# Optimization experiments

Hardware: AMD Instinct MI355X
Metric: run time of the kernel (lower is better)

The kernel has to match this reference:

```python
import jax, jax.numpy as jnp
import numpy as np

EPS = 1e-5


def gated_graph_conv(x, edge_index, W, w_ih, w_hh, b_ih, b_hh):
    # W: [num_layers, C, C]; PyG pads input features up to out_channels C.
    N = x.shape[0]
    C = W.shape[1]
    if x.shape[1] < C:
        x = jnp.pad(x, ((0, 0), (0, C - x.shape[1])))
    src, dst = edge_index[0], edge_index[1]
    for i in range(W.shape[0]):
        m = x @ W[i]                                   # [N, C]
        agg = jax.ops.segment_sum(m[src], dst, num_segments=N)  # scatter-add aggr
        # GRUCell(agg, x)
        gi = agg @ w_ih.T + b_ih                       # [N, 3C]
        gh = x @ w_hh.T + b_hh
        ir, iz, in_ = jnp.split(gi, 3, axis=-1)
        hr, hz, hn = jnp.split(gh, 3, axis=-1)
        r = jax.nn.sigmoid(ir + hr)
        z = jax.nn.sigmoid(iz + hz)
        n = jnp.tanh(in_ + r * hn)
        x = (1.0 - z) * n + z * x
    return x


def batch_norm_eval(x, gamma, beta, mean, var):
    return (x - mean) * jax.lax.rsqrt(var + EPS) * gamma + beta


def _ggc_params(key, C):
    ks = jax.random.split(key, 5)
    s = 1.0 / np.sqrt(C)
    return (jax.random.uniform(ks[0], (4, C, C), minval=-s, maxval=s),
            jax.random.uniform(ks[1], (3 * C, C), minval=-s, maxval=s),
            jax.random.uniform(ks[2], (3 * C, C), minval=-s, maxval=s),
            jax.random.uniform(ks[3], (3 * C,), minval=-s, maxval=s),
            jax.random.uniform(ks[4], (3 * C,), minval=-s, maxval=s))


def _bn_params(key, C):
    ks = jax.random.split(key, 4)
    return (jax.random.normal(ks[0], (C,)) * 0.1 + 1.0,
            jax.random.normal(ks[1], (C,)) * 0.1,
            jax.random.normal(ks[2], (C,)) * 0.1,
            jax.random.uniform(ks[3], (C,), minval=0.5, maxval=1.5))


def setup_inputs() -> dict:
    key = jax.random.key(0)
    N, E, NF, NG, NA = 50000, 800000, 32, 256, 10
    ks = jax.random.split(key, 12)
    x = jax.random.normal(ks[0], (N, NF), dtype=jnp.float32)
    edge_index = jax.random.randint(ks[1], (2, E), 0, N, dtype=jnp.int64)
    batch = jnp.sort(jax.random.randint(ks[2], (N,), 0, NG, dtype=jnp.int64))
    c1 = _ggc_params(ks[3], NF)
    c2 = _ggc_params(ks[4], 64)
    c3 = _ggc_params(ks[5], 128)
    bn1 = _bn_params(ks[6], NF)
    bn2 = _bn_params(ks[7], 64)
    s1 = 1.0 / np.sqrt(128)
    fc1_W = jax.random.uniform(ks[8], (256, 128), minval=-s1, maxval=s1)
    fc1_b = jax.random.uniform(ks[9], (256,), minval=-s1, maxval=s1)
    s2 = 1.0 / np.sqrt(256)
    fc2_W = jax.random.uniform(ks[10], (NA, 256), minval=-s2, maxval=s2)
    fc2_b = jax.random.uniform(ks[11], (NA,), minval=-s2, maxval=s2)
    d = {"x": x, "edge_index": edge_index, "batch": batch,
         "fc1_W": fc1_W, "fc1_b": fc1_b, "fc2_W": fc2_W, "fc2_b": fc2_b}
    for name, p in (("conv1", c1), ("conv2", c2), ("conv3", c3)):
        d[name + "_W"], d[name + "_wih"], d[name + "_whh"], d[name + "_bih"], d[name + "_bhh"] = p
    for name, p in (("bn1", bn1), ("bn2", bn2)):
        d[name + "_gamma"], d[name + "_beta"], d[name + "_mean"], d[name + "_var"] = p
    return d


def reference(x, edge_index, batch,
              conv1_W, conv1_wih, conv1_whh, conv1_bih, conv1_bhh,
              conv2_W, conv2_wih, conv2_whh, conv2_bih, conv2_bhh,
              conv3_W, conv3_wih, conv3_whh, conv3_bih, conv3_bhh,
              bn1_gamma, bn1_beta, bn1_mean, bn1_var,
              bn2_gamma, bn2_beta, bn2_mean, bn2_var,
              fc1_W, fc1_b, fc2_W, fc2_b):
    NUM_GRAPHS = 256
    h = jax.nn.elu(gated_graph_conv(x, edge_index, conv1_W, conv1_wih, conv1_whh, conv1_bih, conv1_bhh))
    h = batch_norm_eval(h, bn1_gamma, bn1_beta, bn1_mean, bn1_var)
    h = jax.nn.elu(gated_graph_conv(h, edge_index, conv2_W, conv2_wih, conv2_whh, conv2_bih, conv2_bhh))
    h = batch_norm_eval(h, bn2_gamma, bn2_beta, bn2_mean, bn2_var)
    h = jax.nn.elu(gated_graph_conv(h, edge_index, conv3_W, conv3_wih, conv3_whh, conv3_bih, conv3_bhh))
    g = jax.ops.segment_sum(h, batch, num_segments=NUM_GRAPHS)  # global_add_pool
    g = jax.nn.elu(g @ fc1_W.T + fc1_b)
    # dropout is identity in eval mode
    return jax.nn.log_softmax(g @ fc2_W.T + fc2_b, axis=-1)
```

## Files before the change

### kernel.cpp

```cpp
#include <hip/hip_runtime.h>
#include <math.h>


#define EPS_BN 1e-5f

typedef short short8 __attribute__((ext_vector_type(8)));
typedef unsigned short u16x8 __attribute__((ext_vector_type(8)));
typedef float f32x4 __attribute__((ext_vector_type(4)));

__device__ __forceinline__ float elu_f(float v) {
    return v > 0.f ? v : expm1f(v);
}
__device__ __forceinline__ float sigmoid_f(float v) {
    return 1.f / (1.f + __expf(-v));
}
__device__ __forceinline__ float tanh_f(float v) {
    float e = __expf(2.f * v);
    return 1.f - 2.f / (e + 1.f);
}
__device__ __forceinline__ unsigned short f2bf(float f) {
    unsigned u = __float_as_uint(f);
    unsigned r = (u + 0x7FFF + ((u >> 16) & 1)) >> 16;
    return (unsigned short)r;
}
__device__ __forceinline__ float bf2f(unsigned short b) {
    return __uint_as_float(((unsigned)b) << 16);
}
__device__ __forceinline__ void put_hl(unsigned short* __restrict__ hi,
                                       unsigned short* __restrict__ lo,
                                       size_t idx, float v) {
    unsigned short h = f2bf(v);
    hi[idx] = h;
    lo[idx] = f2bf(v - bf2f(h));
}


__global__ __launch_bounds__(256) void hist_kernel(
    const int* __restrict__ ei, int* __restrict__ deg, int E) {
    int e = blockIdx.x * 256 + threadIdx.x;
    if (e < E) atomicAdd(&deg[ei[E + e]], 1);
}

__global__ __launch_bounds__(256) void scan1_kernel(
    const int* __restrict__ deg, int* __restrict__ out,
    int* __restrict__ blockSums, int N) {
    __shared__ int sdata[256];
    int b = blockIdx.x, t = threadIdx.x;
    int base = b * 1024 + t * 4;
    int v[4], s = 0;
#pragma unroll
    for (int i = 0; i < 4; ++i) {
        v[i] = (base + i < N) ? deg[base + i] : 0;
        s += v[i];
    }
    sdata[t] = s;
    __syncthreads();
    for (int off = 1; off < 256; off <<= 1) {
        int x = (t >= off) ? sdata[t - off] : 0;
        __syncthreads();
        sdata[t] += x;
        __syncthreads();
    }
    int run = sdata[t] - s;
#pragma unroll
    for (int i = 0; i < 4; ++i) {
        if (base + i < N) out[base + i] = run;
        run += v[i];
    }
    if (t == 255) blockSums[b] = sdata[255];
}

__global__ void scan2_kernel(int* blockSums, int nb) {
    if (threadIdx.x == 0 && blockIdx.x == 0) {
        int run = 0;
        for (int i = 0; i < nb; ++i) {
            int v = blockSums[i];
            blockSums[i] = run;
            run += v;
        }
    }
}

__global__ __launch_bounds__(256) void scan3_kernel(
    const int* __restrict__ out, const int* __restrict__ blockSums,
    int* __restrict__ rowstart, int* __restrict__ writeptr, int N, int E) {
    int i = blockIdx.x * 256 + threadIdx.x;
    if (i < N) {
        int v = out[i] + blockSums[i >> 10];
        rowstart[i] = v;
        writeptr[i] = v;
    }
    if (i == 0) rowstart[N] = E;
}

__global__ __launch_bounds__(256) void fill_kernel(
    const int* __restrict__ ei, int* __restrict__ writeptr,
    int* __restrict__ csr_src, int E) {
    int e = blockIdx.x * 256 + threadIdx.x;
    if (e < E) {
        int d = ei[E + e];
        int p = atomicAdd(&writeptr[d], 1);
        csr_src[p] = ei[e];
    }
}


template <int C>
__global__ __launch_bounds__(256) void wc_kernel(
    const float* __restrict__ W, const float* __restrict__ wih,
    float* __restrict__ Wc) {
    int idx = blockIdx.x * 256 + threadIdx.x;
    if (idx >= 4 * C * 3 * C) return;
    int l = idx / (C * 3 * C);
    int r = idx % (C * 3 * C);
    int k = r / (3 * C);
    int row = r % (3 * C);
    const float* wrow = W + ((size_t)l * C + k) * C;
    const float* irow = wih + (size_t)row * C;
    float acc = 0.f;
#pragma unroll 4
    for (int t = 0; t < C; ++t) acc += wrow[t] * irow[t];
    Wc[idx] = acc;
}


template <int C>
__global__ __launch_bounds__(256) void swizzle_b2_kernel(
    const float* __restrict__ Wc, const float* __restrict__ whh,
    unsigned short* __restrict__ BsHi, unsigned short* __restrict__ BsLo) {
    constexpr int CT = C / 16;
    int idx = blockIdx.x * 256 + threadIdx.x;
    if (idx >= 4 * 6 * C * C) return;
    int l = idx / (6 * C * C);
    int r0 = idx % (6 * C * C);
    int j = r0 & 7;
    int lane = (r0 >> 3) & 63;
    int rest = r0 >> 9;
    int tslot = rest % (3 * CT);
    int ks = rest / (3 * CT);
    int k = ks * 32 + (lane >> 4) * 8 + j;
    int g = tslot / CT;
    int lt = tslot % CT;
    int c = lt * 16 + (lane & 15);
    int row = g * C + c;
    float v = (k < C) ? Wc[((size_t)l * C + k) * 3 * C + row]
                      : whh[(size_t)row * C + (k - C)];
    unsigned short h = f2bf(v);
    BsHi[idx] = h;
    BsLo[idx] = f2bf(v - bf2f(h));
}


template <int C>
__global__ __launch_bounds__(256) void gather_kernel(
    const unsigned short* __restrict__ Xhi,
    const int* __restrict__ rowstart, const int* __restrict__ csr_src,
    unsigned short* __restrict__ Shi, int N) {
    constexpr int LPG = C / 8;
    constexpr int GPB = 256 / LPG;
    int lane = threadIdx.x % LPG;
    int grp = threadIdx.x / LPG;
    int d = blockIdx.x * GPB + grp;
    if (d >= N) return;
    int p = rowstart[d];
    int p1 = rowstart[d + 1];
    float a[8];
#pragma unroll
    for (int j = 0; j < 8; ++j) a[j] = 0.f;
    int off = lane * 8;
    for (; p + 3 < p1; p += 4) {
        int s0 = csr_src[p];
        int s1 = csr_src[p + 1];
        int s2 = csr_src[p + 2];
        int s3 = csr_src[p + 3];
        u16x8 h0 = *(const u16x8*)(Xhi + (size_t)s0 * C + off);
        u16x8 h1 = *(const u16x8*)(Xhi + (size_t)s1 * C + off);
        u16x8 h2 = *(const u16x8*)(Xhi + (size_t)s2 * C + off);
        u16x8 h3 = *(const u16x8*)(Xhi + (size_t)s3 * C + off);
#pragma unroll
        for (int j = 0; j < 8; ++j) {
            a[j] += (bf2f(h0[j]) + bf2f(h1[j])) + (bf2f(h2[j]) + bf2f(h3[j]));
        }
    }
    for (; p < p1; ++p) {
        int s0 = csr_src[p];
        u16x8 h0 = *(const u16x8*)(Xhi + (size_t)s0 * C + off);
#pragma unroll
        for (int j = 0; j < 8; ++j) a[j] += bf2f(h0[j]);
    }
    size_t base = (size_t)d * C + off;
#pragma unroll
    for (int j = 0; j < 8; ++j) Shi[base + j] = f2bf(a[j]);
}


template <int C, int NT, int MINW>
__global__ __launch_bounds__(256, MINW) void gru_mfma_kernel(
    const unsigned short* __restrict__ HinHi, const unsigned short* __restrict__ HinLo,
    unsigned short* __restrict__ HoutHi, unsigned short* __restrict__ HoutLo,
    const unsigned short* __restrict__ Shi,
    const unsigned short* __restrict__ BsHi, const unsigned short* __restrict__ BsLo,
    const float* __restrict__ biasI, const float* __restrict__ biasH, int N) {
    constexpr int CT = C / 16;
    constexpr int KS = C / 16;
    constexpr int CTW = CT / 4;
    constexpr int TPW = NT / 16;
    int wave = threadIdx.x >> 6;
    int lane = threadIdx.x & 63;
    int quad = lane >> 4;
    int l16 = lane & 15;
    int node0 = blockIdx.x * NT;
    int arow[TPW];
#pragma unroll
    for (int t = 0; t < TPW; ++t) {
        int r = node0 + t * 16 + l16;
        arow[t] = r < N ? r : N - 1;
    }
    f32x4 accR[CTW][TPW], accZ[CTW][TPW], accN[CTW][TPW], accH[CTW][TPW];
#pragma unroll
    for (int ct = 0; ct < CTW; ++ct)
#pragma unroll
        for (int t = 0; t < TPW; ++t) {
            accR[ct][t] = (f32x4){0.f, 0.f, 0.f, 0.f};
            accZ[ct][t] = (f32x4){0.f, 0.f, 0.f, 0.f};
            accN[ct][t] = (f32x4){0.f, 0.f, 0.f, 0.f};
            accH[ct][t] = (f32x4){0.f, 0.f, 0.f, 0.f};
        }
    const short8* bhi = (const short8*)BsHi;
    const short8* blo = (const short8*)BsLo;

    for (int ks = 0; ks < KS / 2; ++ks) {
        int k0 = ks * 32 + quad * 8;
        short8 ahi[TPW];
#pragma unroll
        for (int t = 0; t < TPW; ++t)
            ahi[t] = *(const short8*)(Shi + (size_t)arow[t] * C + k0);
#pragma unroll
        for (int ct = 0; ct < CTW; ++ct) {
            int ts = ks * 3 * CT + wave * CTW + ct;
            short8 bhf = bhi[(size_t)ts * 64 + lane];
            short8 blf = blo[(size_t)ts * 64 + lane];
#pragma unroll
            for (int t = 0; t < TPW; ++t) {
                accR[ct][t] = __builtin_amdgcn_mfma_f32_16x16x32_bf16(ahi[t], bhf, accR[ct][t], 0, 0, 0);
                accR[ct][t] = __builtin_amdgcn_mfma_f32_16x16x32_bf16(ahi[t], blf, accR[ct][t], 0, 0, 0);
            }
            bhf = bhi[(size_t)(ts + CT) * 64 + lane];
            blf = blo[(size_t)(ts + CT) * 64 + lane];
#pragma unroll
            for (int t = 0; t < TPW; ++t) {
                accZ[ct][t] = __builtin_amdgcn_mfma_f32_16x16x32_bf16(ahi[t], bhf, accZ[ct][t], 0, 0, 0);
                accZ[ct][t] = __builtin_amdgcn_mfma_f32_16x16x32_bf16(ahi[t], blf, accZ[ct][t], 0, 0, 0);
            }
            bhf = bhi[(size_t)(ts + 2 * CT) * 64 + lane];
            blf = blo[(size_t)(ts + 2 * CT) * 64 + lane];
#pragma unroll
            for (int t = 0; t < TPW; ++t) {
                accN[ct][t] = __builtin_amdgcn_mfma_f32_16x16x32_bf16(ahi[t], bhf, accN[ct][t], 0, 0, 0);
                accN[ct][t] = __builtin_amdgcn_mfma_f32_16x16x32_bf16(ahi[t], blf, accN[ct][t], 0, 0, 0);
            }
        }
    }
    for (int ks = KS / 2; ks < KS; ++ks) {
        int k0 = ks * 32 + quad * 8 - C;
        short8 ahi[TPW], alo[TPW];
#pragma unroll
        for (int t = 0; t < TPW; ++t) {
            ahi[t] = *(const short8*)(HinHi + (size_t)arow[t] * C + k0);
            alo[t] = *(const short8*)(HinLo + (size_t)arow[t] * C + k0);
        }
#pragma unroll
        for (int ct = 0; ct < CTW; ++ct) {
            int ts = ks * 3 * CT + wave * CTW + ct;
            short8 bhf = bhi[(size_t)ts * 64 + lane];
            short8 blf = blo[(size_t)ts * 64 + lane];
#pragma unroll
            for (int t = 0; t < TPW; ++t) {
                accR[ct][t] = __builtin_amdgcn_mfma_f32_16x16x32_bf16(ahi[t], bhf, accR[ct][t], 0, 0, 0);
                accR[ct][t] = __builtin_amdgcn_mfma_f32_16x16x32_bf16(alo[t], bhf, accR[ct][t], 0, 0, 0);
                accR[ct][t] = __builtin_amdgcn_mfma_f32_16x16x32_bf16(ahi[t], blf, accR[ct][t], 0, 0, 0);
            }
            bhf = bhi[(size_t)(ts + CT) * 64 + lane];
            blf = blo[(size_t)(ts + CT) * 64 + lane];
#pragma unroll
            for (int t = 0; t < TPW; ++t) {
                accZ[ct][t] = __builtin_amdgcn_mfma_f32_16x16x32_bf16(ahi[t], bhf, accZ[ct][t], 0, 0, 0);
                accZ[ct][t] = __builtin_amdgcn_mfma_f32_16x16x32_bf16(alo[t], bhf, accZ[ct][t], 0, 0, 0);
                accZ[ct][t] = __builtin_amdgcn_mfma_f32_16x16x32_bf16(ahi[t], blf, accZ[ct][t], 0, 0, 0);
            }
            bhf = bhi[(size_t)(ts + 2 * CT) * 64 + lane];
            blf = blo[(size_t)(ts + 2 * CT) * 64 + lane];
#pragma unroll
            for (int t = 0; t < TPW; ++t) {
                accH[ct][t] = __builtin_amdgcn_mfma_f32_16x16x32_bf16(ahi[t], bhf, accH[ct][t], 0, 0, 0);
                accH[ct][t] = __builtin_amdgcn_mfma_f32_16x16x32_bf16(alo[t], bhf, accH[ct][t], 0, 0, 0);
                accH[ct][t] = __builtin_amdgcn_mfma_f32_16x16x32_bf16(ahi[t], blf, accH[ct][t], 0, 0, 0);
            }
        }
    }

#pragma unroll
    for (int ct = 0; ct < CTW; ++ct) {
        int c = (wave * CTW + ct) * 16 + l16;
        float bir = biasI[c], biz = biasI[C + c], bin = biasI[2 * C + c];
        float bhr = biasH[c], bhz = biasH[C + c], bhn = biasH[2 * C + c];
#pragma unroll
        for (int t = 0; t < TPW; ++t) {
#pragma unroll
            for (int r = 0; r < 4; ++r) {
                int node = node0 + t * 16 + quad * 4 + r;
                if (node < N) {
                    size_t gi = (size_t)node * C + c;
                    float xo = bf2f(HinHi[gi]) + bf2f(HinLo[gi]);
                    float rv = sigmoid_f(accR[ct][t][r] + bir + bhr);
                    float zv = sigmoid_f(accZ[ct][t][r] + biz + bhz);
                    float nv = tanh_f(accN[ct][t][r] + bin + rv * (accH[ct][t][r] + bhn));
                    put_hl(HoutHi, HoutLo, gi, (1.f - zv) * nv + zv * xo);
                }
            }
        }
    }
}

__global__ __launch_bounds__(256, 4) void gru32_kernel(
    const unsigned short* __restrict__ HinHi, const unsigned short* __restrict__ HinLo,
    unsigned short* __restrict__ HoutHi, unsigned short* __restrict__ HoutLo,
    const unsigned short* __restrict__ Shi,
    const unsigned short* __restrict__ BsHi, const unsigned short* __restrict__ BsLo,
    const float* __restrict__ biasI, const float* __restrict__ biasH, int N) {
    constexpr int C = 32;
    constexpr int CT = 2;
    int wave = threadIdx.x >> 6;
    int lane = threadIdx.x & 63;
    int quad = lane >> 4;
    int l16 = lane & 15;
    int node0 = blockIdx.x * 64 + wave * 16;
    int ar = node0 + l16;
    if (ar >= N) ar = N - 1;
    f32x4 accR[CT], accZ[CT], accN[CT], accH[CT];
#pragma unroll
    for (int t = 0; t < CT; ++t) {
        accR[t] = (f32x4){0.f, 0.f, 0.f, 0.f};
        accZ[t] = (f32x4){0.f, 0.f, 0.f, 0.f};
        accN[t] = (f32x4){0.f, 0.f, 0.f, 0.f};
        accH[t] = (f32x4){0.f, 0.f, 0.f, 0.f};
    }
    const short8* bhi = (const short8*)BsHi;
    const short8* blo = (const short8*)BsLo;
    int k0 = quad * 8;
    {
        short8 ahi = *(const short8*)(Shi + (size_t)ar * C + k0);
#pragma unroll
        for (int g = 0; g < 3; ++g) {
            f32x4* acc = g == 0 ? accR : (g == 1 ? accZ : accN);
#pragma unroll
            for (int t = 0; t < CT; ++t) {
                int ts = g * CT + t;
                short8 bhf = bhi[(size_t)ts * 64 + lane];
                short8 blf = blo[(size_t)ts * 64 + lane];
                acc[t] = __builtin_amdgcn_mfma_f32_16x16x32_bf16(ahi, bhf, acc[t], 0, 0, 0);
                acc[t] = __builtin_amdgcn_mfma_f32_16x16x32_bf16(ahi, blf, acc[t], 0, 0, 0);
            }
        }
    }
    {
        short8 ahi = *(const short8*)(HinHi + (size_t)ar * C + k0);
        short8 alo = *(const short8*)(HinLo + (size_t)ar * C + k0);
#pragma unroll
        for (int g = 0; g < 3; ++g) {
            f32x4* acc = g == 0 ? accR : (g == 1 ? accZ : accH);
#pragma unroll
            for (int t = 0; t < CT; ++t) {
                int ts = 3 * CT + g * CT + t;
                short8 bhf = bhi[(size_t)ts * 64 + lane];
                short8 blf = blo[(size_t)ts * 64 + lane];
                acc[t] = __builtin_amdgcn_mfma_f32_16x16x32_bf16(ahi, bhf, acc[t], 0, 0, 0);
                acc[t] = __builtin_amdgcn_mfma_f32_16x16x32_bf16(alo, bhf, acc[t], 0, 0, 0);
                acc[t] = __builtin_amdgcn_mfma_f32_16x16x32_bf16(ahi, blf, acc[t], 0, 0, 0);
            }
        }
    }
#pragma unroll
    for (int t = 0; t < CT; ++t) {
        int c = t * 16 + l16;
        float bir = biasI[c], biz = biasI[C + c], bin = biasI[2 * C + c];
        float bhr = biasH[c], bhz = biasH[C + c], bhn = biasH[2 * C + c];
#pragma unroll
        for (int r = 0; r < 4; ++r) {
            int node = node0 + quad * 4 + r;
            if (node < N) {
                size_t gi = (size_t)node * C + c;
                float xo = bf2f(HinHi[gi]) + bf2f(HinLo[gi]);
                float rv = sigmoid_f(accR[t][r] + bir + bhr);
                float zv = sigmoid_f(accZ[t][r] + biz + bhz);
                float nv = tanh_f(accN[t][r] + bin + rv * (accH[t][r] + bhn));
                put_hl(HoutHi, HoutLo, gi, (1.f - zv) * nv + zv * xo);
            }
        }
    }
}


__global__ __launch_bounds__(256) void init_x_kernel(
    const float* __restrict__ x, unsigned short* __restrict__ Hhi,
    unsigned short* __restrict__ Hlo, int total) {
    int t = blockIdx.x * 256 + threadIdx.x;
    if (t < total) put_hl(Hhi, Hlo, t, x[t]);
}

template <int Cin, int Cout>
__global__ __launch_bounds__(256) void elu_bn_pad_kernel(
    const unsigned short* __restrict__ Shi, const unsigned short* __restrict__ Slo,
    unsigned short* __restrict__ Dhi, unsigned short* __restrict__ Dlo,
    const float* __restrict__ gamma, const float* __restrict__ beta,
    const float* __restrict__ mean, const float* __restrict__ var, int N) {
    long t = (long)blockIdx.x * 256 + threadIdx.x;
    long total = (long)N * Cout;
    if (t >= total) return;
    int n = (int)(t / Cout);
    int c = (int)(t & (Cout - 1));
    float v = 0.f;
    if (c < Cin) {
        size_t si = (size_t)n * Cin + c;
        float x = bf2f(Shi[si]) + bf2f(Slo[si]);
        x = elu_f(x);
        v = (x - mean[c]) * rsqrtf(var[c] + EPS_BN) * gamma[c] + beta[c];
    }
    put_hl(Dhi, Dlo, t, v);
}

__global__ __launch_bounds__(256) void pool_elu_kernel(
    const unsigned short* __restrict__ Hhi, const unsigned short* __restrict__ Hlo,
    const int* __restrict__ batch, float* __restrict__ G, int N) {
    long t = (long)blockIdx.x * 256 + threadIdx.x;
    if (t >= (long)N * 128) return;
    int n = (int)(t >> 7);
    int c = (int)(t & 127);
    float v = elu_f(bf2f(Hhi[t]) + bf2f(Hlo[t]));
    atomicAdd(&G[batch[n] * 128 + c], v);
}

__global__ __launch_bounds__(256) void fc1_kernel(
    const float* __restrict__ G, const float* __restrict__ W,
    const float* __restrict__ b, float* __restrict__ G2) {
    __shared__ float row[128];
    int g = blockIdx.x;
    int j = threadIdx.x;
    if (j < 128) row[j] = G[g * 128 + j];
    __syncthreads();
    float acc = b[j];
    for (int k = 0; k < 128; ++k) acc += row[k] * W[j * 128 + k];
    G2[g * 256 + j] = elu_f(acc);
}

__global__ __launch_bounds__(64) void fc2_logsoftmax_kernel(
    const float* __restrict__ G2, const float* __restrict__ W,
    const float* __restrict__ b, float* __restrict__ out) {
    __shared__ float row[256];
    __shared__ float logits[10];
    __shared__ float red[2];
    int g = blockIdx.x;
    int tid = threadIdx.x;
    for (int i = tid; i < 256; i += 64) row[i] = G2[g * 256 + i];
    __syncthreads();
    if (tid < 10) {
        float acc = b[tid];
        for (int k = 0; k < 256; ++k) acc += row[k] * W[tid * 256 + k];
        logits[tid] = acc;
    }
    __syncthreads();
    if (tid == 0) {
        float m = -1e30f;
        for (int a = 0; a < 10; ++a) m = fmaxf(m, logits[a]);
        float s = 0.f;
        for (int a = 0; a < 10; ++a) s += expf(logits[a] - m);
        red[0] = m;
        red[1] = logf(s);
    }
    __syncthreads();
    if (tid < 10) out[g * 10 + tid] = logits[tid] - red[0] - red[1];
}


template <int C>
static void run_conv(unsigned short* Ahi, unsigned short* Alo,
                     unsigned short* Bhi, unsigned short* Blo,
                     unsigned short* Shi,
                     float* Wc, unsigned short* BsHi, unsigned short* BsLo,
                     const float* W, const float* wih, const float* whh,
                     const float* bih, const float* bhh,
                     const int* rowstart, const int* csr_src,
                     int N, int E, hipStream_t stream) {
    wc_kernel<C><<<(4 * C * 3 * C + 255) / 256, 256, 0, stream>>>(W, wih, Wc);
    swizzle_b2_kernel<C><<<(4 * 6 * C * C + 255) / 256, 256, 0, stream>>>(Wc, whh, BsHi, BsLo);
    constexpr int NT = (C == 128) ? 32 : 64;
    int nb = (N + NT - 1) / NT;
    constexpr int GPB = 2048 / C;
    int gblocks = (N + GPB - 1) / GPB;
    unsigned short *inHi = Ahi, *inLo = Alo, *outHi = Bhi, *outLo = Blo;
    for (int it = 0; it < 4; ++it) {
        gather_kernel<C><<<gblocks, 256, 0, stream>>>(
            inHi, rowstart, csr_src, Shi, N);
        const unsigned short* bs_h = BsHi + (size_t)it * 6 * C * C;
        const unsigned short* bs_l = BsLo + (size_t)it * 6 * C * C;
        if constexpr (C == 32)
            gru32_kernel<<<nb, 256, 0, stream>>>(
                inHi, inLo, outHi, outLo, Shi, bs_h, bs_l, bih, bhh, N);
        else
            gru_mfma_kernel<C, NT, 3><<<nb, 256, 0, stream>>>(
                inHi, inLo, outHi, outLo, Shi, bs_h, bs_l, bih, bhh, N);
        unsigned short* tp;
        tp = inHi; inHi = outHi; outHi = tp;
        tp = inLo; inLo = outLo; outLo = tp;
    }
}

extern "C" void kernel_launch(void* const* d_in, const int* in_sizes, int n_in,
                              void* d_out, int out_size, void* d_ws, size_t ws_size,
                              hipStream_t stream) {
    const float* x = (const float*)d_in[0];
    const int* ei = (const int*)d_in[1];
    const int* batch = (const int*)d_in[2];
    const float* fc1W = (const float*)d_in[3];
    const float* fc1b = (const float*)d_in[4];
    const float* fc2W = (const float*)d_in[5];
    const float* fc2b = (const float*)d_in[6];
    const float* c1W = (const float*)d_in[7];
    const float* c1wih = (const float*)d_in[8];
    const float* c1whh = (const float*)d_in[9];
    const float* c1bih = (const float*)d_in[10];
    const float* c1bhh = (const float*)d_in[11];
    const float* c2W = (const float*)d_in[12];
    const float* c2wih = (const float*)d_in[13];
    const float* c2whh = (const float*)d_in[14];
    const float* c2bih = (const float*)d_in[15];
    const float* c2bhh = (const float*)d_in[16];
    const float* c3W = (const float*)d_in[17];
    const float* c3wih = (const float*)d_in[18];
    const float* c3whh = (const float*)d_in[19];
    const float* c3bih = (const float*)d_in[20];
    const float* c3bhh = (const float*)d_in[21];
    const float* bn1g = (const float*)d_in[22];
    const float* bn1b = (const float*)d_in[23];
    const float* bn1m = (const float*)d_in[24];
    const float* bn1v = (const float*)d_in[25];
    const float* bn2g = (const float*)d_in[26];
    const float* bn2b = (const float*)d_in[27];
    const float* bn2m = (const float*)d_in[28];
    const float* bn2v = (const float*)d_in[29];

    int N = in_sizes[0] / 32;
    int E = in_sizes[1] / 2;

    const size_t NB = (size_t)N * 128;
    unsigned short* PAhi = (unsigned short*)d_ws;
    unsigned short* PAlo = PAhi + NB;
    unsigned short* PBhi = PAlo + NB;
    unsigned short* PBlo = PBhi + NB;
    unsigned short* Shi = PBlo + NB;
    unsigned short* Slo = Shi + NB;
    unsigned short* BsHi = Slo + NB;
    unsigned short* BsLo = BsHi + 393216;
    float* Wc = (float*)(BsLo + 393216);
    float* G = Wc + 196608;
    float* G2 = G + 32768;
    int* deg = (int*)(G2 + 65536);
    int* scanout = deg + N;
    int* rowstart = scanout + N;
    int* writeptr = rowstart + N + 1;
    int* blockSums = writeptr + N;
    int* csr_src = blockSums + 64;

    hipMemsetAsync(deg, 0, (size_t)N * sizeof(int), stream);
    int eblocks = (E + 255) / 256;
    hist_kernel<<<eblocks, 256, 0, stream>>>(ei, deg, E);
    int nscan = (N + 1023) / 1024;
    scan1_kernel<<<nscan, 256, 0, stream>>>(deg, scanout, blockSums, N);
    scan2_kernel<<<1, 64, 0, stream>>>(blockSums, nscan);
    scan3_kernel<<<(N + 255) / 256, 256, 0, stream>>>(scanout, blockSums, rowstart, writeptr, N, E);
    fill_kernel<<<eblocks, 256, 0, stream>>>(ei, writeptr, csr_src, E);

    init_x_kernel<<<(N * 32 + 255) / 256, 256, 0, stream>>>(x, PAhi, PAlo, N * 32);

    run_conv<32>(PAhi, PAlo, PBhi, PBlo, Shi, Wc, BsHi, BsLo,
                 c1W, c1wih, c1whh, c1bih, c1bhh, rowstart, csr_src, N, E, stream);
    elu_bn_pad_kernel<32, 64><<<(int)(((long)N * 64 + 255) / 256), 256, 0, stream>>>(
        PAhi, PAlo, PBhi, PBlo, bn1g, bn1b, bn1m, bn1v, N);

    run_conv<64>(PBhi, PBlo, PAhi, PAlo, Shi, Wc, BsHi, BsLo,
                 c2W, c2wih, c2whh, c2bih, c2bhh, rowstart, csr_src, N, E, stream);
    elu_bn_pad_kernel<64, 128><<<(int)(((long)N * 128 + 255) / 256), 256, 0, stream>>>(
        PBhi, PBlo, PAhi, PAlo, bn2g, bn2b, bn2m, bn2v, N);

    run_conv<128>(PAhi, PAlo, PBhi, PBlo, Shi, Wc, BsHi, BsLo,
                  c3W, c3wih, c3whh, c3bih, c3bhh, rowstart, csr_src, N, E, stream);

    hipMemsetAsync(G, 0, 256 * 128 * sizeof(float), stream);
    pool_elu_kernel<<<(int)(((long)N * 128 + 255) / 256), 256, 0, stream>>>(
        PAhi, PAlo, batch, G, N);

    fc1_kernel<<<256, 256, 0, stream>>>(G, fc1W, fc1b, G2);
    fc2_logsoftmax_kernel<<<256, 64, 0, stream>>>(G2, fc2W, fc2b, (float*)d_out);
}
```

Baseline: 931.0 us.

## Software-pipeline B and A fragment loads in GRU MFMA kernel, retune tiles

Flattens the two k-loops of the GRU MFMA kernel into one fully unrolled loop. B fragments are prefetched three steps ahead through a four-slot register ring, and the A rows for the next k-step are double-buffered, so global load latency overlaps with MFMA work. It also fixes the node tile at 32 for C=64, which was 64 before, and raises min waves per EU to 4 for C=64. The gru32 launch grid is kept unchanged. The cost is higher register pressure and more blocks, with a risk of spills or lower occupancy.

After: 935.1 us. No clear change (+0.4%).

```diff
diff --git a/kernel.cpp b/kernel.cpp
--- a/kernel.cpp
+++ b/kernel.cpp
@@ -194,17 +194,20 @@
 }
 
 
-template <int C, int NT, int MINW>
+template <int C, int MINW>
 __global__ __launch_bounds__(256, MINW) void gru_mfma_kernel(
     const unsigned short* __restrict__ HinHi, const unsigned short* __restrict__ HinLo,
     unsigned short* __restrict__ HoutHi, unsigned short* __restrict__ HoutLo,
     const unsigned short* __restrict__ Shi,
     const unsigned short* __restrict__ BsHi, const unsigned short* __restrict__ BsLo,
     const float* __restrict__ biasI, const float* __restrict__ biasH, int N) {
+    constexpr int NT = 32;
     constexpr int CT = C / 16;
     constexpr int KS = C / 16;
     constexpr int CTW = CT / 4;
     constexpr int TPW = NT / 16;
+    constexpr int JPK = CTW * 3;
+    constexpr int JT = KS * JPK;
     int wave = threadIdx.x >> 6;
     int lane = threadIdx.x & 63;
     int quad = lane >> 4;
@@ -229,72 +232,65 @@
     const short8* bhi = (const short8*)BsHi;
     const short8* blo = (const short8*)BsLo;
 
-    for (int ks = 0; ks < KS / 2; ++ks) {
-        int k0 = ks * 32 + quad * 8;
-        short8 ahi[TPW];
-#pragma unroll
-        for (int t = 0; t < TPW; ++t)
-            ahi[t] = *(const short8*)(Shi + (size_t)arow[t] * C + k0);
-#pragma unroll
-        for (int ct = 0; ct < CTW; ++ct) {
-            int ts = ks * 3 * CT + wave * CTW + ct;
-            short8 bhf = bhi[(size_t)ts * 64 + lane];
-            short8 blf = blo[(size_t)ts * 64 + lane];
+    short8 bufh[4], bufl[4];
+    short8 ahiP[2][TPW], aloP[2][TPW];
+
+    auto loadB = [&](int j) {
+        int ks = j / JPK;
+        int rr = j % JPK;
+        int ct = rr / 3;
+        int g = rr % 3;
+        size_t ts = (size_t)(ks * 3 * CT + wave * CTW + ct + g * CT);
+        bufh[j & 3] = bhi[ts * 64 + lane];
+        bufl[j & 3] = blo[ts * 64 + lane];
+    };
+    auto loadA = [&](int ks) {
+        int slot = ks & 1;
+        if (ks < KS / 2) {
+            int k0 = ks * 32 + quad * 8;
+#pragma unroll
+            for (int t = 0; t < TPW; ++t)
+                ahiP[slot][t] = *(const short8*)(Shi + (size_t)arow[t] * C + k0);
+        } else {
+            int k0 = ks * 32 + quad * 8 - C;
 #pragma unroll
             for (int t = 0; t < TPW; ++t) {
-                accR[ct][t] = __builtin_amdgcn_mfma_f32_16x16x32_bf16(ahi[t], bhf, accR[ct][t], 0, 0, 0);
-                accR[ct][t] = __builtin_amdgcn_mfma_f32_16x16x32_bf16(ahi[t], blf, accR[ct][t], 0, 0, 0);
+                ahiP[slot][t] = *(const short8*)(HinHi + (size_t)arow[t] * C + k0);
+                aloP[slot][t] = *(const short8*)(HinLo + (size_t)arow[t] * C + k0);
             }
-            bhf = bhi[(size_t)(ts + CT) * 64 + lane];
-            blf = blo[(size_t)(ts + CT) * 64 + lane];
+        }
+    };
+
+    loadA(0);
+    loadB(0);
+    loadB(1);
+    loadB(2);
+
+#pragma unroll
+    for (int j = 0; j < JT; ++j) {
+        if (j + 3 < JT) loadB(j + 3);
+        int ks = j / JPK;
+        int rr = j % JPK;
+        int ct = rr / 3;
+        int g = rr % 3;
+        if (rr == 0 && ks + 1 < KS) loadA(ks + 1);
+        int slot = ks & 1;
+        short8 bh = bufh[j & 3];
+        short8 bl = bufl[j & 3];
+        if (ks < KS / 2) {
+            f32x4* acc = (g == 0) ? accR[ct] : (g == 1) ? accZ[ct] : accN[ct];
 #pragma unroll
             for (int t = 0; t < TPW; ++t) {
-                accZ[ct][t] = __builtin_amdgcn_mfma_f32_16x16x32_bf16(ahi[t], bhf, accZ[ct][t], 0, 0, 0);
-                accZ[ct][t] = __builtin_amdgcn_mfma_f32_16x16x32_bf16(ahi[t], blf, accZ[ct][t], 0, 0, 0);
+                acc[t] = __builtin_amdgcn_mfma_f32_16x16x32_bf16(ahiP[slot][t], bh, acc[t], 0, 0, 0);
+                acc[t] = __builtin_amdgcn_mfma_f32_16x16x32_bf16(ahiP[slot][t], bl, acc[t], 0, 0, 0);
             }
-            bhf = bhi[(size_t)(ts + 2 * CT) * 64 + lane];
-            blf = blo[(size_t)(ts + 2 * CT) * 64 + lane];
+        } else {
+            f32x4* acc = (g == 0) ? accR[ct] : (g == 1) ? accZ[ct] : accH[ct];
 #pragma unroll
             for (int t = 0; t < TPW; ++t) {
-                accN[ct][t] = __builtin_amdgcn_mfma_f32_16x16x32_bf16(ahi[t], bhf, accN[ct][t], 0, 0, 0);
-                accN[ct][t] = __builtin_amdgcn_mfma_f32_16x16x32_bf16(ahi[t], blf, accN[ct][t], 0, 0, 0);
-            }
-        }
-    }
-    for (int ks = KS / 2; ks < KS; ++ks) {
-        int k0 = ks * 32 + quad * 8 - C;
-        short8 ahi[TPW], alo[TPW];
-#pragma unroll
-        for (int t = 0; t < TPW; ++t) {
-            ahi[t] = *(const short8*)(HinHi + (size_t)arow[t] * C + k0);
-            alo[t] = *(const short8*)(HinLo + (size_t)arow[t] * C + k0);
-        }
-#pragma unroll
-        for (int ct = 0; ct < CTW; ++ct) {
-            int ts = ks * 3 * CT + wave * CTW + ct;
-            short8 bhf = bhi[(size_t)ts * 64 + lane];
-            short8 blf = blo[(size_t)ts * 64 + lane];
-#pragma unroll
-            for (int t = 0; t < TPW; ++t) {
-                accR[ct][t] = __builtin_amdgcn_mfma_f32_16x16x32_bf16(ahi[t], bhf, accR[ct][t], 0, 0, 0);
-                accR[ct][t] = __builtin_amdgcn_mfma_f32_16x16x32_bf16(alo[t], bhf, accR[ct][t], 0, 0, 0);
-                accR[ct][t] = __builtin_amdgcn_mfma_f32_16x16x32_bf16(ahi[t], blf, accR[ct][t], 0, 0, 0);
-            }
-            bhf = bhi[(size_t)(ts + CT) * 64 + lane];
-            blf = blo[(size_t)(ts + CT) * 64 + lane];
-#pragma unroll
-            for (int t = 0; t < TPW; ++t) {
-                accZ[ct][t] = __builtin_amdgcn_mfma_f32_16x16x32_bf16(ahi[t], bhf, accZ[ct][t], 0, 0, 0);
-                accZ[ct][t] = __builtin_amdgcn_mfma_f32_16x16x32_bf16(alo[t], bhf, accZ[ct][t], 0, 0, 0);
-                accZ[ct][t] = __builtin_amdgcn_mfma_f32_16x16x32_bf16(ahi[t], blf, accZ[ct][t], 0, 0, 0);
-            }
-            bhf = bhi[(size_t)(ts + 2 * CT) * 64 + lane];
-            blf = blo[(size_t)(ts + 2 * CT) * 64 + lane];
-#pragma unroll
-            for (int t = 0; t < TPW; ++t) {
-                accH[ct][t] = __builtin_amdgcn_mfma_f32_16x16x32_bf16(ahi[t], bhf, accH[ct][t], 0, 0, 0);
-                accH[ct][t] = __builtin_amdgcn_mfma_f32_16x16x32_bf16(alo[t], bhf, accH[ct][t], 0, 0, 0);
-                accH[ct][t] = __builtin_amdgcn_mfma_f32_16x16x32_bf16(ahi[t], blf, accH[ct][t], 0, 0, 0);
+                acc[t] = __builtin_amdgcn_mfma_f32_16x16x32_bf16(ahiP[slot][t], bh, acc[t], 0, 0, 0);
+                acc[t] = __builtin_amdgcn_mfma_f32_16x16x32_bf16(aloP[slot][t], bh, acc[t], 0, 0, 0);
+                acc[t] = __builtin_amdgcn_mfma_f32_16x16x32_bf16(ahiP[slot][t], bl, acc[t], 0, 0, 0);
             }
         }
     }
@@ -493,7 +489,7 @@
                      int N, int E, hipStream_t stream) {
     wc_kernel<C><<<(4 * C * 3 * C + 255) / 256, 256, 0, stream>>>(W, wih, Wc);
     swizzle_b2_kernel<C><<<(4 * 6 * C * C + 255) / 256, 256, 0, stream>>>(Wc, whh, BsHi, BsLo);
-    constexpr int NT = (C == 128) ? 32 : 64;
+    constexpr int NT = 32;
     int nb = (N + NT - 1) / NT;
     constexpr int GPB = 2048 / C;
     int gblocks = (N + GPB - 1) / GPB;
@@ -504,10 +500,10 @@
         const unsigned short* bs_h = BsHi + (size_t)it * 6 * C * C;
         const unsigned short* bs_l = BsLo + (size_t)it * 6 * C * C;
         if constexpr (C == 32)
-            gru32_kernel<<<nb, 256, 0, stream>>>(
+            gru32_kernel<<<(N + 63) / 64, 256, 0, stream>>>(
                 inHi, inLo, outHi, outLo, Shi, bs_h, bs_l, bih, bhh, N);
         else
-            gru_mfma_kernel<C, NT, 3><<<nb, 256, 0, stream>>>(
+            gru_mfma_kernel<C, (C == 128 ? 3 : 4)><<<nb, 256, 0, stream>>>(
                 inHi, inLo, outHi, outLo, Shi, bs_h, bs_l, bih, bhh, N);
         unsigned short* tp;
         tp = inHi; inHi = outHi; outHi = tp;
```

## Stage GRU weight tiles into LDS with double-buffered async global-to-LDS loads

Applied to the files above, without the earlier changes.

The GRU MFMA kernel now copies each k-step's hi/lo weight tiles into shared memory using global_load_lds and double buffers them. Each block reads the B fragments from LDS while the next k-slice is prefetched, so the four waves no longer each fetch their weight slices straight from global memory. Tiles grow to 64 nodes per block for C=128 as well, and occupancy hints drop to 1 for C=128 and 2 for C=64. The cost is a barrier per k-step, a large LDS footprint (96KB per block for C=128), and higher register pressure from the larger tile, all of which can lower occupancy.

Result: slower. 1.016 ms (+9.1%).

```diff
diff --git a/kernel.cpp b/kernel.cpp
--- a/kernel.cpp
+++ b/kernel.cpp
@@ -32,6 +32,12 @@
     unsigned short h = f2bf(v);
     hi[idx] = h;
     lo[idx] = f2bf(v - bf2f(h));
+}
+
+__device__ __forceinline__ void gl_lds16(const void* g, void* l) {
+    __builtin_amdgcn_global_load_lds(
+        (const __attribute__((address_space(1))) unsigned int*)g,
+        (__attribute__((address_space(3))) unsigned int*)l, 16, 0, 0);
 }
 
 
@@ -194,8 +200,8 @@
 }
 
 
-template <int C, int NT, int MINW>
-__global__ __launch_bounds__(256, MINW) void gru_mfma_kernel(
+template <int C, int MINW>
+__global__ __launch_bounds__(256, MINW) void gru_lds_kernel(
     const unsigned short* __restrict__ HinHi, const unsigned short* __restrict__ HinLo,
     unsigned short* __restrict__ HoutHi, unsigned short* __restrict__ HoutLo,
     const unsigned short* __restrict__ Shi,
@@ -204,12 +210,16 @@
     constexpr int CT = C / 16;
     constexpr int KS = C / 16;
     constexpr int CTW = CT / 4;
-    constexpr int TPW = NT / 16;
+    constexpr int TPW = 4;
+    constexpr int CHUNKS = 3 * CT;
+    constexpr int SKB = CHUNKS * 1024;
+    __shared__ char ldsB[2][2][SKB];
+
     int wave = threadIdx.x >> 6;
     int lane = threadIdx.x & 63;
     int quad = lane >> 4;
     int l16 = lane & 15;
-    int node0 = blockIdx.x * NT;
+    int node0 = blockIdx.x * 64;
     int arow[TPW];
 #pragma unroll
     for (int t = 0; t < TPW; ++t) {
@@ -226,77 +236,65 @@
             accN[ct][t] = (f32x4){0.f, 0.f, 0.f, 0.f};
             accH[ct][t] = (f32x4){0.f, 0.f, 0.f, 0.f};
         }
-    const short8* bhi = (const short8*)BsHi;
-    const short8* blo = (const short8*)BsLo;
-
-    for (int ks = 0; ks < KS / 2; ++ks) {
-        int k0 = ks * 32 + quad * 8;
-        short8 ahi[TPW];
-#pragma unroll
-        for (int t = 0; t < TPW; ++t)
-            ahi[t] = *(const short8*)(Shi + (size_t)arow[t] * C + k0);
+
+    auto stage = [&](int ks, int buf) {
+        const char* gh = (const char*)BsHi + (size_t)ks * SKB;
+        const char* gl = (const char*)BsLo + (size_t)ks * SKB;
+#pragma unroll
+        for (int i = 0; i < CHUNKS / 4; ++i) {
+            int c = i * 4 + wave;
+            gl_lds16(gh + (size_t)c * 1024 + (size_t)lane * 16, &ldsB[buf][0][c * 1024]);
+            gl_lds16(gl + (size_t)c * 1024 + (size_t)lane * 16, &ldsB[buf][1][c * 1024]);
+        }
+    };
+
+    stage(0, 0);
+    __syncthreads();
+
+#pragma unroll
+    for (int ks = 0; ks < KS; ++ks) {
+        const int buf = ks & 1;
+        if (ks + 1 < KS) stage(ks + 1, buf ^ 1);
+        short8 ahi[TPW], alo[TPW];
+        if (ks < KS / 2) {
+            int k0 = ks * 32 + quad * 8;
+#pragma unroll
+            for (int t = 0; t < TPW; ++t)
+                ahi[t] = *(const short8*)(Shi + (size_t)arow[t] * C + k0);
+        } else {
+            int k0 = ks * 32 + quad * 8 - C;
+#pragma unroll
+            for (int t = 0; t < TPW; ++t) {
+                ahi[t] = *(const short8*)(HinHi + (size_t)arow[t] * C + k0);
+                alo[t] = *(const short8*)(HinLo + (size_t)arow[t] * C + k0);
+            }
+        }
 #pragma unroll
         for (int ct = 0; ct < CTW; ++ct) {
-            int ts = ks * 3 * CT + wave * CTW + ct;
-            short8 bhf = bhi[(size_t)ts * 64 + lane];
-            short8 blf = blo[(size_t)ts * 64 + lane];
-#pragma unroll
-            for (int t = 0; t < TPW; ++t) {
-                accR[ct][t] = __builtin_amdgcn_mfma_f32_16x16x32_bf16(ahi[t], bhf, accR[ct][t], 0, 0, 0);
-                accR[ct][t] = __builtin_amdgcn_mfma_f32_16x16x32_bf16(ahi[t], blf, accR[ct][t], 0, 0, 0);
+#pragma unroll
+            for (int g = 0; g < 3; ++g) {
+                int tl = g * CT + wave * CTW + ct;
+                short8 bh = *(const short8*)&ldsB[buf][0][tl * 1024 + lane * 16];
+                short8 bl = *(const short8*)&ldsB[buf][1][tl * 1024 + lane * 16];
+                if (ks < KS / 2) {
+                    f32x4* acc = (g == 0) ? accR[ct] : (g == 1) ? accZ[ct] : accN[ct];
+#pragma unroll
+                    for (int t = 0; t < TPW; ++t) {
+                        acc[t] = __builtin_amdgcn_mfma_f32_16x16x32_bf16(ahi[t], bh, acc[t], 0, 0, 0);
+                        acc[t] = __builtin_amdgcn_mfma_f32_16x16x32_bf16(ahi[t], bl, acc[t], 0, 0, 0);
+                    }
+                } else {
+                    f32x4* acc = (g == 0) ? accR[ct] : (g == 1) ? accZ[ct] : accH[ct];
+#pragma unroll
+                    for (int t = 0; t < TPW; ++t) {
+                        acc[t] = __builtin_amdgcn_mfma_f32_16x16x32_bf16(ahi[t], bh, acc[t], 0, 0, 0);
+                        acc[t] = __builtin_amdgcn_mfma_f32_16x16x32_bf16(alo[t], bh, acc[t], 0, 0, 0);
+                        acc[t] = __builtin_amdgcn_mfma_f32_16x16x32_bf16(ahi[t], bl, acc[t], 0, 0, 0);
+                    }
+                }
             }
-            bhf = bhi[(size_t)(ts + CT) * 64 + lane];
-            blf = blo[(size_t)(ts + CT) * 64 + lane];
-#pragma unroll
-            for (int t = 0; t < TPW; ++t) {
-                accZ[ct][t] = __builtin_amdgcn_mfma_f32_16x16x32_bf16(ahi[t], bhf, accZ[ct][t], 0, 0, 0);
-                accZ[ct][t] = __builtin_amdgcn_mfma_f32_16x16x32_bf16(ahi[t], blf, accZ[ct][t], 0, 0, 0);
-            }
-            bhf = bhi[(size_t)(ts + 2 * CT) * 64 + lane];
-            blf = blo[(size_t)(ts + 2 * CT) * 64 + lane];
-#pragma unroll
-            for (int t = 0; t < TPW; ++t) {
-                accN[ct][t] = __builtin_amdgcn_mfma_f32_16x16x32_bf16(ahi[t], bhf, accN[ct][t], 0, 0, 0);
-                accN[ct][t] = __builtin_amdgcn_mfma_f32_16x16x32_bf16(ahi[t], blf, accN[ct][t], 0, 0, 0);
-            }
-        }
-    }
-    for (int ks = KS / 2; ks < KS; ++ks) {
-        int k0 = ks * 32 + quad * 8 - C;
-        short8 ahi[TPW], alo[TPW];
-#pragma unroll
-        for (int t = 0; t < TPW; ++t) {
-            ahi[t] = *(const short8*)(HinHi + (size_t)arow[t] * C + k0);
-            alo[t] = *(const short8*)(HinLo + (size_t)arow[t] * C + k0);
-        }
-#pragma unroll
-        for (int ct = 0; ct < CTW; ++ct) {
-            int ts = ks * 3 * CT + wave * CTW + ct;
-            short8 bhf = bhi[(size_t)ts * 64 + lane];
-            short8 blf = blo[(size_t)ts * 64 + lane];
-#pragma unroll
-            for (int t = 0; t < TPW; ++t) {
-                accR[ct][t] = __builtin_amdgcn_mfma_f32_16x16x32_bf16(ahi[t], bhf, accR[ct][t], 0, 0, 0);
-                accR[ct][t] = __builtin_amdgcn_mfma_f32_16x16x32_bf16(alo[t], bhf, accR[ct][t], 0, 0, 0);
-                accR[ct][t] = __builtin_amdgcn_mfma_f32_16x16x32_bf16(ahi[t], blf, accR[ct][t], 0, 0, 0);
-            }
-            bhf = bhi[(size_t)(ts + CT) * 64 + lane];
-            blf = blo[(size_t)(ts + CT) * 64 + lane];
-#pragma unroll
-            for (int t = 0; t < TPW; ++t) {
-                accZ[ct][t] = __builtin_amdgcn_mfma_f32_16x16x32_bf16(ahi[t], bhf, accZ[ct][t], 0, 0, 0);
-                accZ[ct][t] = __builtin_amdgcn_mfma_f32_16x16x32_bf16(alo[t], bhf, accZ[ct][t], 0, 0, 0);
-                accZ[ct][t] = __builtin_amdgcn_mfma_f32_16x16x32_bf16(ahi[t], blf, accZ[ct][t], 0, 0, 0);
-            }
-            bhf = bhi[(size_t)(ts + 2 * CT) * 64 + lane];
-            blf = blo[(size_t)(ts + 2 * CT) * 64 + lane];
-#pragma unroll
-            for (int t = 0; t < TPW; ++t) {
-                accH[ct][t] = __builtin_amdgcn_mfma_f32_16x16x32_bf16(ahi[t], bhf, accH[ct][t], 0, 0, 0);
-                accH[ct][t] = __builtin_amdgcn_mfma_f32_16x16x32_bf16(alo[t], bhf, accH[ct][t], 0, 0, 0);
-                accH[ct][t] = __builtin_amdgcn_mfma_f32_16x16x32_bf16(ahi[t], blf, accH[ct][t], 0, 0, 0);
-            }
-        }
+        }
+        __syncthreads();
     }
 
 #pragma unroll
@@ -493,8 +491,7 @@
                      int N, int E, hipStream_t stream) {
     wc_kernel<C><<<(4 * C * 3 * C + 255) / 256, 256, 0, stream>>>(W, wih, Wc);
     swizzle_b2_kernel<C><<<(4 * 6 * C * C + 255) / 256, 256, 0, stream>>>(Wc, whh, BsHi, BsLo);
-    constexpr int NT = (C == 128) ? 32 : 64;
-    int nb = (N + NT - 1) / NT;
+    int nb = (N + 63) / 64;
     constexpr int GPB = 2048 / C;
     int gblocks = (N + GPB - 1) / GPB;
     unsigned short *inHi = Ahi, *inLo = Alo, *outHi = Bhi, *outLo = Blo;
@@ -507,7 +504,7 @@
             gru32_kernel<<<nb, 256, 0, stream>>>(
                 inHi, inLo, outHi, outLo, Shi, bs_h, bs_l, bih, bhh, N);
         else
-            gru_mfma_kernel<C, NT, 3><<<nb, 256, 0, stream>>>(
+            gru_lds_kernel<C, (C == 128 ? 1 : 2)><<<nb, 256, 0, stream>>>(
                 inHi, inLo, outHi, outLo, Shi, bs_h, bs_l, bih, bhh, N);
         unsigned short* tp;
         tp = inHi; inHi = outHi; outHi = tp;
```

## Overlap gather and GRU stages by splitting nodes into two halves

Applied to the files above, without the earlier changes.

Each gated-graph iteration is split into three launches over two node halves. The first launch gathers the first half. The second interleaves blocks that gather the second half with GRU blocks for the first half, and the third runs the GRU on the second half. The goal is to overlap the memory-bound neighbour gather with the MFMA-heavy GRU, and to fill the GPU better than two serialised kernels do. In exchange it adds a launch per iteration, and mixing block types in one launch can hurt occupancy, because the combined kernel carries the GRU's register budget.

Result: slower. 1.061 ms (+14.0%).

```diff
diff --git a/kernel.cpp b/kernel.cpp
--- a/kernel.cpp
+++ b/kernel.cpp
@@ -152,16 +152,15 @@
 
 
 template <int C>
-__global__ __launch_bounds__(256) void gather_kernel(
+__device__ __forceinline__ void gather_dev(
     const unsigned short* __restrict__ Xhi,
     const int* __restrict__ rowstart, const int* __restrict__ csr_src,
-    unsigned short* __restrict__ Shi, int N) {
+    unsigned short* __restrict__ Shi, int d0, int d1) {
     constexpr int LPG = C / 8;
-    constexpr int GPB = 256 / LPG;
     int lane = threadIdx.x % LPG;
     int grp = threadIdx.x / LPG;
-    int d = blockIdx.x * GPB + grp;
-    if (d >= N) return;
+    int d = d0 + grp;
+    if (d >= d1) return;
     int p = rowstart[d];
     int p1 = rowstart[d + 1];
     float a[8];
@@ -193,28 +192,27 @@
     for (int j = 0; j < 8; ++j) Shi[base + j] = f2bf(a[j]);
 }
 
-
-template <int C, int NT, int MINW>
-__global__ __launch_bounds__(256, MINW) void gru_mfma_kernel(
+template <int C>
+__device__ __forceinline__ void gru_dev(
     const unsigned short* __restrict__ HinHi, const unsigned short* __restrict__ HinLo,
     unsigned short* __restrict__ HoutHi, unsigned short* __restrict__ HoutLo,
     const unsigned short* __restrict__ Shi,
     const unsigned short* __restrict__ BsHi, const unsigned short* __restrict__ BsLo,
-    const float* __restrict__ biasI, const float* __restrict__ biasH, int N) {
+    const float* __restrict__ biasI, const float* __restrict__ biasH,
+    int node0, int nlim) {
     constexpr int CT = C / 16;
     constexpr int KS = C / 16;
     constexpr int CTW = CT / 4;
-    constexpr int TPW = NT / 16;
+    constexpr int TPW = 2;
     int wave = threadIdx.x >> 6;
     int lane = threadIdx.x & 63;
     int quad = lane >> 4;
     int l16 = lane & 15;
-    int node0 = blockIdx.x * NT;
     int arow[TPW];
 #pragma unroll
     for (int t = 0; t < TPW; ++t) {
         int r = node0 + t * 16 + l16;
-        arow[t] = r < N ? r : N - 1;
+        arow[t] = r < nlim ? r : nlim - 1;
     }
     f32x4 accR[CTW][TPW], accZ[CTW][TPW], accN[CTW][TPW], accH[CTW][TPW];
 #pragma unroll
@@ -309,7 +307,7 @@
 #pragma unroll
             for (int r = 0; r < 4; ++r) {
                 int node = node0 + t * 16 + quad * 4 + r;
-                if (node < N) {
+                if (node < nlim) {
                     size_t gi = (size_t)node * C + c;
                     float xo = bf2f(HinHi[gi]) + bf2f(HinLo[gi]);
                     float rv = sigmoid_f(accR[ct][t][r] + bir + bhr);
@@ -322,21 +320,47 @@
     }
 }
 
-__global__ __launch_bounds__(256, 4) void gru32_kernel(
+
+template <int C, int MINW>
+__global__ __launch_bounds__(256, MINW) void combo_kernel(
+    const unsigned short* __restrict__ HinHi, const unsigned short* __restrict__ HinLo,
+    unsigned short* __restrict__ HoutHi, unsigned short* __restrict__ HoutLo,
+    unsigned short* __restrict__ Shi,
+    const int* __restrict__ rowstart, const int* __restrict__ csr_src,
+    const unsigned short* __restrict__ BsHi, const unsigned short* __restrict__ BsLo,
+    const float* __restrict__ biasI, const float* __restrict__ biasH,
+    int g_d0, int g_d1, int r_n0, int r_n1, int gb, int tb) {
+    constexpr int GPB = 2048 / C;
+    long bid = blockIdx.x;
+    long a = ((bid + 1) * (long)gb) / tb;
+    long b = (bid * (long)gb) / tb;
+    if (a > b) {
+        gather_dev<C>(HinHi, rowstart, csr_src, Shi,
+                      g_d0 + (int)b * GPB, g_d1);
+    } else {
+        int ridx = (int)(bid - a);
+        gru_dev<C>(HinHi, HinLo, HoutHi, HoutLo, Shi, BsHi, BsLo,
+                   biasI, biasH, r_n0 + ridx * 32, r_n1);
+    }
+}
+
+
+__device__ __forceinline__ void gru32_dev(
     const unsigned short* __restrict__ HinHi, const unsigned short* __restrict__ HinLo,
     unsigned short* __restrict__ HoutHi, unsigned short* __restrict__ HoutLo,
     const unsigned short* __restrict__ Shi,
     const unsigned short* __restrict__ BsHi, const unsigned short* __restrict__ BsLo,
-    const float* __restrict__ biasI, const float* __restrict__ biasH, int N) {
+    const float* __restrict__ biasI, const float* __restrict__ biasH,
+    int blk0, int nlim) {
     constexpr int C = 32;
     constexpr int CT = 2;
     int wave = threadIdx.x >> 6;
     int lane = threadIdx.x & 63;
     int quad = lane >> 4;
     int l16 = lane & 15;
-    int node0 = blockIdx.x * 64 + wave * 16;
+    int node0 = blk0 + wave * 16;
     int ar = node0 + l16;
-    if (ar >= N) ar = N - 1;
+    if (ar >= nlim) ar = nlim - 1;
     f32x4 accR[CT], accZ[CT], accN[CT], accH[CT];
 #pragma unroll
     for (int t = 0; t < CT; ++t) {
@@ -388,7 +412,7 @@
 #pragma unroll
         for (int r = 0; r < 4; ++r) {
             int node = node0 + quad * 4 + r;
-            if (node < N) {
+            if (node < nlim) {
                 size_t gi = (size_t)node * C + c;
                 float xo = bf2f(HinHi[gi]) + bf2f(HinLo[gi]);
                 float rv = sigmoid_f(accR[t][r] + bir + bhr);
@@ -397,6 +421,28 @@
                 put_hl(HoutHi, HoutLo, gi, (1.f - zv) * nv + zv * xo);
             }
         }
+    }
+}
+
+__global__ __launch_bounds__(256, 4) void combo32_kernel(
+    const unsigned short* __restrict__ HinHi, const unsigned short* __restrict__ HinLo,
+    unsigned short* __restrict__ HoutHi, unsigned short* __restrict__ HoutLo,
+    unsigned short* __restrict__ Shi,
+    const int* __restrict__ rowstart, const int* __restrict__ csr_src,
+    const unsigned short* __restrict__ BsHi, const unsigned short* __restrict__ BsLo,
+    const float* __restrict__ biasI, const float* __restrict__ biasH,
+    int g_d0, int g_d1, int r_n0, int r_n1, int gb, int tb) {
+    constexpr int GPB = 64;
+    long bid = blockIdx.x;
+    long a = ((bid + 1) * (long)gb) / tb;
+    long b = (bid * (long)gb) / tb;
+    if (a > b) {
+        gather_dev<32>(HinHi, rowstart, csr_src, Shi,
+                       g_d0 + (int)b * GPB, g_d1);
+    } else {
+        int ridx = (int)(bid - a);
+        gru32_dev(HinHi, HinLo, HoutHi, HoutLo, Shi, BsHi, BsLo,
+                  biasI, biasH, r_n0 + ridx * 64, r_n1);
     }
 }
 
@@ -493,22 +539,39 @@
                      int N, int E, hipStream_t stream) {
     wc_kernel<C><<<(4 * C * 3 * C + 255) / 256, 256, 0, stream>>>(W, wih, Wc);
     swizzle_b2_kernel<C><<<(4 * 6 * C * C + 255) / 256, 256, 0, stream>>>(Wc, whh, BsHi, BsLo);
-    constexpr int NT = (C == 128) ? 32 : 64;
-    int nb = (N + NT - 1) / NT;
     constexpr int GPB = 2048 / C;
-    int gblocks = (N + GPB - 1) / GPB;
+    constexpr int NT = (C == 32) ? 64 : 32;
+    int h1 = ((N / 2 + 63) / 64) * 64;
+    if (h1 > N) h1 = N;
+    int gb1 = (h1 + GPB - 1) / GPB;
+    int gb2 = (N - h1 + GPB - 1) / GPB;
+    int rb1 = (h1 + NT - 1) / NT;
+    int rb2 = (N - h1 + NT - 1) / NT;
     unsigned short *inHi = Ahi, *inLo = Alo, *outHi = Bhi, *outLo = Blo;
     for (int it = 0; it < 4; ++it) {
-        gather_kernel<C><<<gblocks, 256, 0, stream>>>(
-            inHi, rowstart, csr_src, Shi, N);
         const unsigned short* bs_h = BsHi + (size_t)it * 6 * C * C;
         const unsigned short* bs_l = BsLo + (size_t)it * 6 * C * C;
-        if constexpr (C == 32)
-            gru32_kernel<<<nb, 256, 0, stream>>>(
-                inHi, inLo, outHi, outLo, Shi, bs_h, bs_l, bih, bhh, N);
-        else
-            gru_mfma_kernel<C, NT, 3><<<nb, 256, 0, stream>>>(
-                inHi, inLo, outHi, outLo, Shi, bs_h, bs_l, bih, bhh, N);
+        if constexpr (C == 32) {
+            combo32_kernel<<<gb1, 256, 0, stream>>>(
+                inHi, inLo, outHi, outLo, Shi, rowstart, csr_src, bs_h, bs_l,
+                bih, bhh, 0, h1, 0, 0, gb1, gb1);
+            combo32_kernel<<<gb2 + rb1, 256, 0, stream>>>(
+                inHi, inLo, outHi, outLo, Shi, rowstart, csr_src, bs_h, bs_l,
+                bih, bhh, h1, N, 0, h1, gb2, gb2 + rb1);
+            combo32_kernel<<<rb2, 256, 0, stream>>>(
+                inHi, inLo, outHi, outLo, Shi, rowstart, csr_src, bs_h, bs_l,
+                bih, bhh, 0, 0, h1, N, 0, rb2);
+        } else {
+            combo_kernel<C, 3><<<gb1, 256, 0, stream>>>(
+                inHi, inLo, outHi, outLo, Shi, rowstart, csr_src, bs_h, bs_l,
+                bih, bhh, 0, h1, 0, 0, gb1, gb1);
+            combo_kernel<C, 3><<<gb2 + rb1, 256, 0, stream>>>(
+                inHi, inLo, outHi, outLo, Shi, rowstart, csr_src, bs_h, bs_l,
+                bih, bhh, h1, N, 0, h1, gb2, gb2 + rb1);
+            combo_kernel<C, 3><<<rb2, 256, 0, stream>>>(
+                inHi, inLo, outHi, outLo, Shi, rowstart, csr_src, bs_h, bs_l,
+                bih, bhh, 0, 0, h1, N, 0, rb2);
+        }
         unsigned short* tp;
         tp = inHi; inHi = outHi; outHi = tp;
         tp = inLo; inLo = outLo; outLo = tp;
```
